# Kernel optimization log

Measured on AMD Instinct MI355X. Metric: run time of the kernel, lower is better.

Reference implementation:

```python
import jax, jax.numpy as jnp
import numpy as np

PAD_TOKEN = 0.0
REPLACEMENT_PROB = 0.1


def setup_inputs() -> dict:
    key = jax.random.key(0)
    # item-ID-like values in [0, 100000); zeros act as pad tokens
    x = jax.random.randint(key, (16384, 2048), 0, 100000).astype(jnp.float32)
    return {"x": x}


def reference(x):
    """Stochastic Swap Noise: replace ~p of non-pad positions with values
    sampled without replacement from the non-pad values of the tensor.

    Jit-friendly equivalent of torch's
      bernoulli -> masked_select compaction -> randperm -> scatter
    chain: a single argsort on random keys (pads keyed to +2.0) both
    compacts the non-pad values to the front AND shuffles them; a cumsum
    over the replacement mask assigns each replaced position its donor.
    """
    key = jax.random.key(42)
    k_bern, k_shuf = jax.random.split(key)

    nonpad = x != PAD_TOKEN                                        # [B,S] bool
    repl = (jax.random.uniform(k_bern, x.shape) < REPLACEMENT_PROB) & nonpad

    flat_x = x.reshape(-1)                                          # [N]
    flat_nonpad = nonpad.reshape(-1)
    flat_repl = repl.reshape(-1)

    # compaction + shuffle in one sort: non-pad elems get uniform [0,1) keys,
    # pads get 2.0 so they sink to the end.
    r = jnp.where(flat_nonpad, jax.random.uniform(k_shuf, flat_x.shape), 2.0)
    order = jnp.argsort(r)
    donors = flat_x[order]                                          # shuffled non-pad values first

    # k-th replaced position (in flat order) takes donors[k]
    rank = jnp.cumsum(flat_repl) - 1                                # -1 where not replaced (masked out below)
    out = jnp.where(flat_repl, donors[rank], flat_x)
    return out.reshape(x.shape)
```

## Files before the change

### kernel.cpp

```cpp
#include <hip/hip_runtime.h>
#include <stdint.h>

static __host__ __device__ inline uint32_t rotl32(uint32_t x, int r) {
  return (x << r) | (x >> (32 - r));
}

static __host__ __device__ inline void tf2x32(uint32_t k0, uint32_t k1,
                                              uint32_t x0, uint32_t x1,
                                              uint32_t& o0, uint32_t& o1) {
  uint32_t k2 = k0 ^ k1 ^ 0x1BD11BDAu;
#define TFR(a) { x0 += x1; x1 = rotl32(x1, a); x1 ^= x0; }
  x0 += k0; x1 += k1;
  TFR(13) TFR(15) TFR(26) TFR(6)
  x0 += k1; x1 += k2 + 1u;
  TFR(17) TFR(29) TFR(16) TFR(24)
  x0 += k2; x1 += k0 + 2u;
  TFR(13) TFR(15) TFR(26) TFR(6)
  x0 += k0; x1 += k1 + 3u;
  TFR(17) TFR(29) TFR(16) TFR(24)
  x0 += k1; x1 += k2 + 4u;
  TFR(13) TFR(15) TFR(26) TFR(6)
  x0 += k2; x1 += k0 + 5u;
#undef TFR
  o0 = x0; o1 = x1;
}

static __device__ inline uint32_t fold_bits(uint32_t k0, uint32_t k1, uint32_t ctr) {
  uint32_t a, b;
  tf2x32(k0, k1, 0u, ctr, a, b);
  return a ^ b;
}

#define CUT2      917504u
#define NBINS2    896u
#define NH        1024
#define ELEMS_G   8192
#define GPOOL     1216u
#define BSCAP     4608u
#define WIN       8192
#define CAPDUMP   3932160u
#define STRIDE    4608u
#define MASKI     0x07FFFFFFu
#define BERN_THR  838861u


template<bool BOUNDS>
__global__ __launch_bounds__(256) void k_gen(const float* __restrict__ x,
                                             uint64_t* __restrict__ mask,
                                             uint32_t* __restrict__ rsums,
                                             uint32_t* __restrict__ dumpCursor,
                                             uint2* __restrict__ dump,
                                             uint32_t bk0, uint32_t bk1,
                                             uint32_t sk0, uint32_t sk1, int n) {
  __shared__ uint2 pool[GPOOL];
  __shared__ uint32_t wcnt[4];
  __shared__ uint32_t lpoolCnt, lgbase;
  int tid = threadIdx.x, lane = tid & 63, wid = tid >> 6;
  int base = blockIdx.x * ELEMS_G;
  if (tid == 0) lpoolCnt = 0;
  __syncthreads();

  uint32_t cnt = 0;
  for (int k = 0; k < ELEMS_G / 256; k++) {
    int i = base + k * 256 + tid;
    bool inb = !BOUNDS || (i < n);
    float xv = inb ? x[i] : 0.0f;
    bool nonpad = (xv != 0.0f) && inb;
    uint32_t bb = fold_bits(bk0, bk1, (uint32_t)i);
    bool r = nonpad && ((bb >> 9) < BERN_THR);
    unsigned long long ball = __ballot(r);
    int wword = (base + k * 256 + wid * 64) >> 6;
    if (lane == 0 && (!BOUNDS || wword * 64 < n)) mask[wword] = (uint64_t)ball;
    cnt += r ? 1u : 0u;
    uint32_t mm = fold_bits(sk0, sk1, (uint32_t)i) >> 9;
    if (nonpad && mm < CUT2) {
      uint32_t slot = atomicAdd(&lpoolCnt, 1u);
      uint32_t v = (uint32_t)xv;
      if (slot < GPOOL)
        pool[slot] = make_uint2((mm << 12) | (v >> 5), ((v & 31u) << 27) | (uint32_t)i);
    }
  }
  for (int d = 32; d >= 1; d >>= 1) cnt += __shfl_down(cnt, d, 64);
  if (lane == 0) wcnt[wid] = cnt;
  __syncthreads();
  if (tid == 0) {
    rsums[blockIdx.x] = wcnt[0] + wcnt[1] + wcnt[2] + wcnt[3];
    uint32_t pc = lpoolCnt; if (pc > GPOOL) pc = GPOOL;
    lgbase = atomicAdd((unsigned int*)dumpCursor, pc);
  }
  __syncthreads();
  uint32_t pc = lpoolCnt; if (pc > GPOOL) pc = GPOOL;
  uint32_t gb = lgbase;
  for (uint32_t j = tid; j < pc; j += 256) {
    uint32_t d = gb + j;
    if (d < CAPDUMP) dump[d] = pool[j];
  }
}

__global__ void k_scan_single(uint32_t* __restrict__ data, int n) {
  __shared__ uint32_t wsum[4];
  int tid = threadIdx.x, lane = tid & 63, wid = tid >> 6;
  uint32_t running = 0;
  for (int base = 0; base < n; base += 256) {
    int i = base + tid;
    uint32_t v = (i < n) ? data[i] : 0u;
    uint32_t incl = v;
    for (int d = 1; d < 64; d <<= 1) {
      uint32_t t = __shfl_up(incl, (unsigned)d, 64);
      if (lane >= d) incl += t;
    }
    if (lane == 63) wsum[wid] = incl;
    __syncthreads();
    uint32_t woff = 0, tot = 0;
    for (int w = 0; w < 4; w++) { uint32_t s = wsum[w]; if (w < wid) woff += s; tot += s; }
    if (i < n) data[i] = running + woff + (incl - v);
    running += tot;
    __syncthreads();
  }
  if (tid == 0) data[n] = running;
}

__global__ __launch_bounds__(256) void k_regroup(const uint2* __restrict__ dump,
                                                 const uint32_t* __restrict__ dumpCursor,
                                                 uint32_t* __restrict__ fineCursor,
                                                 uint2* __restrict__ fine) {
  __shared__ uint2    pool2[WIN];
  __shared__ uint32_t lhist[NH];
  __shared__ uint32_t lgbase[NH];
  __shared__ uint32_t wsums[4];
  int tid = threadIdx.x, lane = tid & 63, wid = tid >> 6;
  uint32_t total = dumpCursor[0];
  if (total > CAPDUMP) total = CAPDUMP;
  uint32_t wbase = blockIdx.x * (uint32_t)WIN;
  if (wbase >= total) return;
  uint32_t valid = total - wbase;
  if (valid > WIN) valid = WIN;

  for (int b = tid; b < NH; b += 256) lhist[b] = 0;
  __syncthreads();
  uint2 e[WIN / 256];
#pragma unroll
  for (int q = 0; q < WIN / 256; q++) {
    uint32_t j = (uint32_t)q * 256u + (uint32_t)tid;
    e[q] = (j < valid) ? dump[wbase + j] : make_uint2(0u, 0u);
    if (j < valid) atomicAdd(&lhist[e[q].x >> 22], 1u);
  }
  __syncthreads();
  for (int b = tid; b < NH; b += 256) {
    uint32_t h = lhist[b];
    lgbase[b] = h ? atomicAdd((unsigned int*)&fineCursor[b], h) : 0u;
  }
  __syncthreads();
  uint32_t h0 = lhist[4 * tid], h1 = lhist[4 * tid + 1],
           h2 = lhist[4 * tid + 2], h3 = lhist[4 * tid + 3];
  uint32_t tsum = h0 + h1 + h2 + h3;
  uint32_t incl = tsum;
  for (int d = 1; d < 64; d <<= 1) {
    uint32_t t = __shfl_up(incl, (unsigned)d, 64);
    if (lane >= d) incl += t;
  }
  if (lane == 63) wsums[wid] = incl;
  __syncthreads();
  if (wid == 0) {
    uint32_t v = (lane < 4) ? wsums[lane] : 0u;
    uint32_t in2 = v;
    for (int d = 1; d < 4; d <<= 1) {
      uint32_t t = __shfl_up(in2, (unsigned)d, 64);
      if (lane >= d) in2 += t;
    }
    if (lane < 4) wsums[lane] = in2 - v;
  }
  __syncthreads();
  uint32_t texcl = wsums[wid] + (incl - tsum);
  uint32_t e0 = texcl, e1 = e0 + h0, e2 = e1 + h1, e3 = e2 + h2;
  __syncthreads();
  lhist[4 * tid] = e0; lhist[4 * tid + 1] = e1;
  lhist[4 * tid + 2] = e2; lhist[4 * tid + 3] = e3;
  __syncthreads();
#pragma unroll
  for (int q = 0; q < WIN / 256; q++) {
    uint32_t j = (uint32_t)q * 256u + (uint32_t)tid;
    if (j < valid) {
      uint32_t b = e[q].x >> 22;
      uint32_t lpos = atomicAdd(&lhist[b], 1u);
      pool2[lpos] = e[q];
    }
  }
  __syncthreads();
  for (uint32_t j = tid; j < valid; j += 256) {
    uint2 p = pool2[j];
    uint32_t b = p.x >> 22;
    uint32_t st = (b == 0) ? 0u : lhist[b - 1];
    uint32_t dst = lgbase[b] + (j - st);
    if (dst < STRIDE) fine[(size_t)b * STRIDE + dst] = p;
  }
}

__global__ __launch_bounds__(256) void k_binsort(const uint2* __restrict__ pairs,
                                                 const uint32_t* __restrict__ binPrefix,
                                                 float* __restrict__ donors) {
  __shared__ uint2    lbuf[BSCAP];
  __shared__ uint32_t hist[NH];
  __shared__ uint32_t wsums[4];
  int tid = threadIdx.x, lane = tid & 63, wid = tid >> 6;
  uint32_t bin = blockIdx.x;
  uint32_t gbase = binPrefix[bin];
  uint32_t cnt = binPrefix[bin + 1] - gbase;
  if (cnt > STRIDE) cnt = STRIDE;
  if (cnt > BSCAP) cnt = BSCAP;
  const uint2* src = pairs + (size_t)bin * STRIDE;

  for (int c = tid; c < 1024; c += 256) hist[c] = 0;
  __syncthreads();
  for (uint32_t j = tid; j < cnt; j += 256)
    atomicAdd(&hist[(src[j].x >> 12) & 1023u], 1u);
  __syncthreads();
  uint32_t h0 = hist[4 * tid], h1 = hist[4 * tid + 1],
           h2 = hist[4 * tid + 2], h3 = hist[4 * tid + 3];
  uint32_t tsum = h0 + h1 + h2 + h3;
  uint32_t incl = tsum;
  for (int d = 1; d < 64; d <<= 1) {
    uint32_t t = __shfl_up(incl, (unsigned)d, 64);
    if (lane >= d) incl += t;
  }
  if (lane == 63) wsums[wid] = incl;
  __syncthreads();
  if (wid == 0) {
    uint32_t v = (lane < 4) ? wsums[lane] : 0u;
    uint32_t in2 = v;
    for (int d = 1; d < 4; d <<= 1) {
      uint32_t t = __shfl_up(in2, (unsigned)d, 64);
      if (lane >= d) in2 += t;
    }
    if (lane < 4) wsums[lane] = in2 - v;
  }
  __syncthreads();
  uint32_t texcl = wsums[wid] + (incl - tsum);
  uint32_t e0 = texcl, e1 = e0 + h0, e2 = e1 + h1, e3 = e2 + h2;
  __syncthreads();
  hist[4 * tid] = e0; hist[4 * tid + 1] = e1;
  hist[4 * tid + 2] = e2; hist[4 * tid + 3] = e3;
  __syncthreads();
  for (uint32_t j = tid; j < cnt; j += 256) {
    uint2 p = src[j];
    uint32_t c = (p.x >> 12) & 1023u;
    uint32_t lpos = atomicAdd(&hist[c], 1u);
    lbuf[lpos] = p;
  }
  __syncthreads();
  for (int c = tid; c < 1024; c += 256) {
    uint32_t lo = (c == 0) ? 0u : hist[c - 1];
    uint32_t hi = hist[c];
    for (uint32_t u = lo + 1; u < hi; u++) {
      uint2 v = lbuf[u];
      uint32_t w = u;
      while (w > lo && (lbuf[w - 1].y & MASKI) > (v.y & MASKI)) {
        lbuf[w] = lbuf[w - 1];
        w--;
      }
      lbuf[w] = v;
    }
  }
  __syncthreads();
  for (uint32_t j = tid; j < cnt; j += 256) {
    uint2 p = lbuf[j];
    uint32_t v = ((p.x & 0xFFFu) << 5) | (p.y >> 27);
    donors[gbase + j] = (float)v;
  }
}

template<bool BOUNDS>
__global__ __launch_bounds__(256) void k_final(const float* __restrict__ x,
                                               const uint64_t* __restrict__ mask,
                                               const uint32_t* __restrict__ rsums,
                                               const float* __restrict__ donors,
                                               float* __restrict__ out, int n) {
  __shared__ uint64_t lwords[ELEMS_G / 64];
  __shared__ uint32_t pcS[ELEMS_G / 64];
  __shared__ uint32_t spanS[4];
  int tid = threadIdx.x, lane = tid & 63, wid = tid >> 6;
  int base = blockIdx.x * ELEMS_G;
  int wordBase = base >> 6;
  if (tid < ELEMS_G / 64) {
    uint64_t w = (!BOUNDS || (size_t)(wordBase + tid) * 64 < (size_t)n)
                     ? mask[wordBase + tid] : 0ull;
    lwords[tid] = w;
    pcS[tid] = (uint32_t)__popcll(w);
  }
  __syncthreads();
  if (tid < 4) {
    uint32_t s = 0;
    for (int q = 0; q < 32; q++) s += pcS[tid * 32 + q];
    spanS[tid] = s;
  }
  __syncthreads();
  uint32_t running = rsums[blockIdx.x];
  for (int w = 0; w < 4; w++) { if (w < wid) running += spanS[w]; }
  for (int k = 0; k < 32; k++) {
    int lw = wid * 32 + k;
    uint64_t word = lwords[lw];
    int i = base + lw * 64 + lane;
    bool r = (word >> lane) & 1ull;
    uint32_t inword = (uint32_t)__popcll(word & ((1ull << lane) - 1ull));
    if (!BOUNDS || i < n) {
      float o = x[i];
      if (r) o = donors[running + inword];
      out[i] = o;
    }
    running += (uint32_t)__popcll(word);
  }
}

extern "C" void kernel_launch(void* const* d_in, const int* in_sizes, int n_in,
                              void* d_out, int out_size, void* d_ws, size_t ws_size,
                              hipStream_t stream) {
  const float* x = (const float*)d_in[0];
  float* out = (float*)d_out;
  int n = in_sizes[0];
  (void)n_in; (void)out_size; (void)ws_size;

  uint32_t bk0, bk1, sk0, sk1;
  tf2x32(0u, 42u, 0u, 0u, bk0, bk1);
  tf2x32(0u, 42u, 0u, 1u, sk0, sk1);

  int nBlkG = (n + ELEMS_G - 1) / ELEMS_G;
  bool exact = ((n % ELEMS_G) == 0);

  size_t off = 0;
  auto alloc = [&](size_t bytes) -> void* {
    void* p = (uint8_t*)d_ws + off;
    off += (bytes + 255) & ~(size_t)255;
    return p;
  };
  uint32_t* dumpCursor = (uint32_t*)alloc(4);
  uint32_t* fineCursor = (uint32_t*)alloc((size_t)(NH + 1) * 4);
  uint32_t* rsums      = (uint32_t*)alloc((size_t)(nBlkG + 1) * 4);
  uint64_t* mask       = (uint64_t*)alloc((size_t)((n + 63) / 64) * 8);
  uint2*    dump       = (uint2*)alloc((size_t)CAPDUMP * 8);
  uint2*    fine       = (uint2*)alloc((size_t)NBINS2 * STRIDE * 8);
  float*    donors     = (float*)dump;

  hipMemsetAsync(dumpCursor, 0, (size_t)(NH + 2) * 4 + 512, stream);

  if (exact)
    k_gen<false><<<nBlkG, 256, 0, stream>>>(x, mask, rsums, dumpCursor, dump,
                                            bk0, bk1, sk0, sk1, n);
  else
    k_gen<true><<<nBlkG, 256, 0, stream>>>(x, mask, rsums, dumpCursor, dump,
                                           bk0, bk1, sk0, sk1, n);
  k_scan_single<<<1, 256, 0, stream>>>(rsums, nBlkG);
  int nWin = (int)((CAPDUMP + WIN - 1) / WIN);
  k_regroup<<<nWin, 256, 0, stream>>>(dump, dumpCursor, fineCursor, fine);
  k_scan_single<<<1, 256, 0, stream>>>(fineCursor, (int)NBINS2);
  k_binsort<<<(int)NBINS2, 256, 0, stream>>>(fine, fineCursor, donors);
  if (exact)
    k_final<false><<<nBlkG, 256, 0, stream>>>(x, mask, rsums, donors, out, n);
  else
    k_final<true><<<nBlkG, 256, 0, stream>>>(x, mask, rsums, donors, out, n);
}
```

Measured before the change: 355.8 us.

## Vectorize gen and final kernels with float4 loads and interleaved mask layout

k_gen and k_final now have each lane handle four consecutive elements through float4 loads and stores instead of one scalar element per iteration. To make that work, the replacement bitmask is stored in an interleaved layout: each 256-element chunk holds four ballot words, one per vector component. k_final decodes ranks from this layout using per-chunk prefix counts. The goal is fewer, wider memory transactions on the two bandwidth-bound passes, at the cost of a more complex rank computation.

```diff
diff --git a/kernel.cpp b/kernel.cpp
--- a/kernel.cpp
+++ b/kernel.cpp
@@ -44,6 +44,7 @@
 #define BERN_THR  838861u
 
 
+
 template<bool BOUNDS>
 __global__ __launch_bounds__(256) void k_gen(const float* __restrict__ x,
                                              uint64_t* __restrict__ mask,
@@ -61,23 +62,46 @@
   __syncthreads();
 
   uint32_t cnt = 0;
-  for (int k = 0; k < ELEMS_G / 256; k++) {
-    int i = base + k * 256 + tid;
-    bool inb = !BOUNDS || (i < n);
-    float xv = inb ? x[i] : 0.0f;
-    bool nonpad = (xv != 0.0f) && inb;
-    uint32_t bb = fold_bits(bk0, bk1, (uint32_t)i);
-    bool r = nonpad && ((bb >> 9) < BERN_THR);
-    unsigned long long ball = __ballot(r);
-    int wword = (base + k * 256 + wid * 64) >> 6;
-    if (lane == 0 && (!BOUNDS || wword * 64 < n)) mask[wword] = (uint64_t)ball;
-    cnt += r ? 1u : 0u;
-    uint32_t mm = fold_bits(sk0, sk1, (uint32_t)i) >> 9;
-    if (nonpad && mm < CUT2) {
-      uint32_t slot = atomicAdd(&lpoolCnt, 1u);
-      uint32_t v = (uint32_t)xv;
-      if (slot < GPOOL)
-        pool[slot] = make_uint2((mm << 12) | (v >> 5), ((v & 31u) << 27) | (uint32_t)i);
+  unsigned long long bball[4];
+  for (int it = 0; it < ELEMS_G / 1024; it++) {
+    int e0 = base + it * 1024 + wid * 256 + lane * 4;
+    float4 xv;
+    if (!BOUNDS || e0 + 3 < n) {
+      xv = *reinterpret_cast<const float4*>(x + e0);
+    } else {
+      xv.x = (e0 + 0 < n) ? x[e0 + 0] : 0.0f;
+      xv.y = (e0 + 1 < n) ? x[e0 + 1] : 0.0f;
+      xv.z = (e0 + 2 < n) ? x[e0 + 2] : 0.0f;
+      xv.w = (e0 + 3 < n) ? x[e0 + 3] : 0.0f;
+    }
+#define GENE(e, comp)                                                     \
+    {                                                                     \
+      uint32_t ii = (uint32_t)(e0 + e);                                   \
+      bool np = (comp != 0.0f);                                           \
+      uint32_t bb = fold_bits(bk0, bk1, ii);                              \
+      bool rr = np && ((bb >> 9) < BERN_THR);                             \
+      bball[e] = __ballot(rr);                                            \
+      cnt += rr ? 1u : 0u;                                                \
+      uint32_t mm = fold_bits(sk0, sk1, ii) >> 9;                         \
+      if (np && mm < CUT2) {                                              \
+        uint32_t slot = atomicAdd(&lpoolCnt, 1u);                         \
+        uint32_t v = (uint32_t)comp;                                      \
+        if (slot < GPOOL)                                                 \
+          pool[slot] = make_uint2((mm << 12) | (v >> 5),                  \
+                                  ((v & 31u) << 27) | ii);                \
+      }                                                                   \
+    }
+    GENE(0, xv.x) GENE(1, xv.y) GENE(2, xv.z) GENE(3, xv.w)
+#undef GENE
+    if (lane == 0) {
+      uint32_t ci = (uint32_t)blockIdx.x * 32u + (uint32_t)it * 4u + (uint32_t)wid;
+      if (!BOUNDS) {
+        mask[ci * 4 + 0] = bball[0]; mask[ci * 4 + 1] = bball[1];
+        mask[ci * 4 + 2] = bball[2]; mask[ci * 4 + 3] = bball[3];
+      } else {
+        for (int e = 0; e < 4; e++)
+          if ((int)(ci * 256u + (uint32_t)e * 64u) < n) mask[ci * 4 + e] = bball[e];
+      }
     }
   }
   for (int d = 32; d >= 1; d >>= 1) cnt += __shfl_down(cnt, d, 64);
@@ -275,39 +299,63 @@
                                                const uint32_t* __restrict__ rsums,
                                                const float* __restrict__ donors,
                                                float* __restrict__ out, int n) {
-  __shared__ uint64_t lwords[ELEMS_G / 64];
-  __shared__ uint32_t pcS[ELEMS_G / 64];
-  __shared__ uint32_t spanS[4];
+  __shared__ uint64_t lw[ELEMS_G / 64];
+  __shared__ uint32_t ctot[32], cpre[32];
   int tid = threadIdx.x, lane = tid & 63, wid = tid >> 6;
   int base = blockIdx.x * ELEMS_G;
-  int wordBase = base >> 6;
+  int wordBase = blockIdx.x * (ELEMS_G / 64);
   if (tid < ELEMS_G / 64) {
-    uint64_t w = (!BOUNDS || (size_t)(wordBase + tid) * 64 < (size_t)n)
-                     ? mask[wordBase + tid] : 0ull;
-    lwords[tid] = w;
-    pcS[tid] = (uint32_t)__popcll(w);
-  }
-  __syncthreads();
-  if (tid < 4) {
-    uint32_t s = 0;
-    for (int q = 0; q < 32; q++) s += pcS[tid * 32 + q];
-    spanS[tid] = s;
-  }
-  __syncthreads();
-  uint32_t running = rsums[blockIdx.x];
-  for (int w = 0; w < 4; w++) { if (w < wid) running += spanS[w]; }
-  for (int k = 0; k < 32; k++) {
-    int lw = wid * 32 + k;
-    uint64_t word = lwords[lw];
-    int i = base + lw * 64 + lane;
-    bool r = (word >> lane) & 1ull;
-    uint32_t inword = (uint32_t)__popcll(word & ((1ull << lane) - 1ull));
-    if (!BOUNDS || i < n) {
-      float o = x[i];
-      if (r) o = donors[running + inword];
-      out[i] = o;
-    }
-    running += (uint32_t)__popcll(word);
+    uint64_t w = 0ull;
+    int wI = wordBase + tid;
+    if (!BOUNDS || (((wI >> 2) * 256) + ((wI & 3) * 64) < n)) w = mask[wI];
+    lw[tid] = w;
+  }
+  __syncthreads();
+  if (tid < 32) {
+    ctot[tid] = (uint32_t)(__popcll(lw[4 * tid]) + __popcll(lw[4 * tid + 1]) +
+                           __popcll(lw[4 * tid + 2]) + __popcll(lw[4 * tid + 3]));
+  }
+  __syncthreads();
+  if (tid == 0) {
+    uint32_t run = 0;
+    for (int c = 0; c < 32; c++) { cpre[c] = run; run += ctot[c]; }
+  }
+  __syncthreads();
+  uint32_t rbase = rsums[blockIdx.x];
+  uint64_t lt = (1ull << lane) - 1ull;
+  for (int it = 0; it < ELEMS_G / 1024; it++) {
+    int c = it * 4 + wid;
+    uint64_t b0 = lw[c * 4 + 0], b1 = lw[c * 4 + 1],
+             b2 = lw[c * 4 + 2], b3 = lw[c * 4 + 3];
+    uint32_t running = rbase + cpre[c];
+    int e0 = base + it * 1024 + wid * 256 + lane * 4;
+    uint32_t below = (uint32_t)(__popcll(b0 & lt) + __popcll(b1 & lt) +
+                                __popcll(b2 & lt) + __popcll(b3 & lt));
+    uint32_t r0 = (uint32_t)((b0 >> lane) & 1ull), r1 = (uint32_t)((b1 >> lane) & 1ull);
+    uint32_t r2 = (uint32_t)((b2 >> lane) & 1ull), r3 = (uint32_t)((b3 >> lane) & 1ull);
+    uint32_t rk = running + below;
+    float4 xv;
+    if (!BOUNDS || e0 + 3 < n) {
+      xv = *reinterpret_cast<const float4*>(x + e0);
+    } else {
+      xv.x = (e0 + 0 < n) ? x[e0 + 0] : 0.0f;
+      xv.y = (e0 + 1 < n) ? x[e0 + 1] : 0.0f;
+      xv.z = (e0 + 2 < n) ? x[e0 + 2] : 0.0f;
+      xv.w = (e0 + 3 < n) ? x[e0 + 3] : 0.0f;
+    }
+    float4 ov;
+    ov.x = r0 ? donors[rk] : xv.x;               rk += r0;
+    ov.y = r1 ? donors[rk] : xv.y;               rk += r1;
+    ov.z = r2 ? donors[rk] : xv.z;               rk += r2;
+    ov.w = r3 ? donors[rk] : xv.w;
+    if (!BOUNDS || e0 + 3 < n) {
+      *reinterpret_cast<float4*>(out + e0) = ov;
+    } else {
+      if (e0 + 0 < n) out[e0 + 0] = ov.x;
+      if (e0 + 1 < n) out[e0 + 1] = ov.y;
+      if (e0 + 2 < n) out[e0 + 2] = ov.z;
+      if (e0 + 3 < n) out[e0 + 3] = ov.w;
+    }
   }
 }
 
@@ -335,7 +383,7 @@
   uint32_t* dumpCursor = (uint32_t*)alloc(4);
   uint32_t* fineCursor = (uint32_t*)alloc((size_t)(NH + 1) * 4);
   uint32_t* rsums      = (uint32_t*)alloc((size_t)(nBlkG + 1) * 4);
-  uint64_t* mask       = (uint64_t*)alloc((size_t)((n + 63) / 64) * 8);
+  uint64_t* mask       = (uint64_t*)alloc((size_t)((n + 63) / 64 + 4) * 8);
   uint2*    dump       = (uint2*)alloc((size_t)CAPDUMP * 8);
   uint2*    fine       = (uint2*)alloc((size_t)NBINS2 * STRIDE * 8);
   float*    donors     = (float*)dump;
```

Result: faster. 339.0 us (-4.7%).
